# Performance work log

Measured on AMD Instinct MI355X. Metric: run time of the kernel, lower is better.

## Reference

```python
import jax, jax.numpy as jnp
import numpy as np

H = 6  # hidden size == input size

def setup_inputs() -> dict:
    key = jax.random.key(0)
    ks = jax.random.split(key, 14)
    B, T = 8192, 512
    s_in = 1.0 / np.sqrt(H)
    inp = {
        "x": jax.random.normal(ks[0], (B, T, H), dtype=jnp.float32),
        # PyTorch LSTM param layout: w_ih [4H, in], w_hh [4H, H], gate order i,f,g,o
        "w_ih_0": jax.random.uniform(ks[1], (4 * H, H), jnp.float32, -s_in, s_in),
        "w_hh_0": jax.random.uniform(ks[2], (4 * H, H), jnp.float32, -s_in, s_in),
        "b_ih_0": jax.random.uniform(ks[3], (4 * H,), jnp.float32, -s_in, s_in),
        "b_hh_0": jax.random.uniform(ks[4], (4 * H,), jnp.float32, -s_in, s_in),
        "w_ih_1": jax.random.uniform(ks[5], (4 * H, H), jnp.float32, -s_in, s_in),
        "w_hh_1": jax.random.uniform(ks[6], (4 * H, H), jnp.float32, -s_in, s_in),
        "b_ih_1": jax.random.uniform(ks[7], (4 * H,), jnp.float32, -s_in, s_in),
        "b_hh_1": jax.random.uniform(ks[8], (4 * H,), jnp.float32, -s_in, s_in),
        "fc1_w": jax.random.uniform(ks[9], (32, H), jnp.float32, -s_in, s_in),
        "fc1_b": jax.random.uniform(ks[10], (32,), jnp.float32, -s_in, s_in),
        "fc2_w": jax.random.uniform(ks[11], (1, 32), jnp.float32, -1 / np.sqrt(32), 1 / np.sqrt(32)),
        "fc2_b": jax.random.uniform(ks[12], (1,), jnp.float32, -1 / np.sqrt(32), 1 / np.sqrt(32)),
    }
    return inp


def _lstm_cell(x_t, h, c, w_ih, w_hh, b):
    # gates: [B, 4H]; PyTorch order i, f, g, o
    gates = x_t @ w_ih.T + h @ w_hh.T + b
    i, f, g, o = jnp.split(gates, 4, axis=-1)
    i = jax.nn.sigmoid(i)
    f = jax.nn.sigmoid(f)
    g = jnp.tanh(g)
    o = jax.nn.sigmoid(o)
    c_new = f * c + i * g
    h_new = o * jnp.tanh(c_new)
    return h_new, c_new


def reference(x, w_ih_0, w_hh_0, b_ih_0, b_hh_0, w_ih_1, w_hh_1, b_ih_1, b_hh_1,
              fc1_w, fc1_b, fc2_w, fc2_b):
    B, T, _ = x.shape
    b0 = b_ih_0 + b_hh_0
    b1 = b_ih_1 + b_hh_1
    zeros = jnp.zeros((B, H), dtype=x.dtype)

    def step(carry, x_t):
        h0, c0, h1, c1 = carry
        h0, c0 = _lstm_cell(x_t, h0, c0, w_ih_0, w_hh_0, b0)
        h1, c1 = _lstm_cell(h0, h1, c1, w_ih_1, w_hh_1, b1)
        return (h0, c0, h1, c1), h1

    xs = jnp.swapaxes(x, 0, 1)  # [T, B, H]
    _, ys = jax.lax.scan(step, (zeros, zeros, zeros, zeros), xs)
    out = jnp.swapaxes(ys, 0, 1)  # [B, T, H]

    # eval-mode: dropout is identity
    out = jax.nn.relu(out @ fc1_w.T + fc1_b)
    out = jax.nn.relu(out @ fc2_w.T + fc2_b)
    return out  # [B, T, 1]
```

## Files before the change

### kernel.cpp

```cpp
#include <hip/hip_runtime.h>


typedef float v2f __attribute__((ext_vector_type(2)));

static constexpr float L2E  = 1.44269504088896340736f;
static constexpr float TL2E = 2.0f * L2E;

#define DPP_QP(a,b,c,d) ((a)|((b)<<2)|((c)<<4)|((d)<<6))
#define DPP_X1  DPP_QP(1,0,3,2)
#define DPP_X2  DPP_QP(2,3,0,1)
#define DPP_B0  DPP_QP(0,0,0,0)
#define DPP_B1  DPP_QP(1,1,1,1)
#define DPP_B2  DPP_QP(2,2,2,2)
#define DPP_B3  DPP_QP(3,3,3,3)
#define DPP_X8  0x128

template<int CTRL>
__device__ __forceinline__ float dppf(float v) {
    return __int_as_float(__builtin_amdgcn_update_dpp(
        0, __float_as_int(v), CTRL, 0xF, 0xF, true));
}

#define PIN(v) asm volatile("" : "+v"(v))

#define PKFMA_LO(d,a,b) asm("v_pk_fma_f32 %0, %1, %2, %0 op_sel:[0,0,0] op_sel_hi:[1,0,1]" : "+v"(d) : "v"(a), "v"(b))
#define PKFMA_HI(d,a,b) asm("v_pk_fma_f32 %0, %1, %2, %0 op_sel:[0,1,0] op_sel_hi:[1,1,1]" : "+v"(d) : "v"(a), "v"(b))
#define PKADD(d,a,b)    asm("v_pk_add_f32 %0, %1, %2" : "=v"(d) : "v"(a), "v"(b))

__device__ __forceinline__ float sig_pre(float a) {
    return __builtin_amdgcn_rcpf(1.0f + __builtin_amdgcn_exp2f(a));
}
__device__ __forceinline__ float tanh_pre(float a) {
    return fmaf(-2.0f, __builtin_amdgcn_rcpf(1.0f + __builtin_amdgcn_exp2f(a)), 1.0f);
}

extern "C" __global__ void __launch_bounds__(64)
__attribute__((amdgpu_waves_per_eu(1, 1)))
lstm_dpp8v6(const float* __restrict__ x,
            const float* __restrict__ wih0, const float* __restrict__ whh0,
            const float* __restrict__ bih0, const float* __restrict__ bhh0,
            const float* __restrict__ wih1, const float* __restrict__ whh1,
            const float* __restrict__ bih1, const float* __restrict__ bhh1,
            const float* __restrict__ fc1w, const float* __restrict__ fc1b,
            const float* __restrict__ fc2w, const float* __restrict__ fc2b,
            float* __restrict__ out, int nbatch)
{
    const int L   = threadIdx.x;
    const int l   = L & 15;
    const int row = L >> 4;
    const int cst = (l >> 2) & 1;
    const int p   = (l & 3) | ((l >> 3) << 2);
    const bool lowq = ((L >> 3) & 1) == 0;

    int seq = blockIdx.x * 8 + row * 2 + cst;
    const bool live = (seq < nbatch);
    if (!live) seq = nbatch - 1;

    const float km = (p < 6) ? 1.0f : 0.0f;
    const int   k  = (p < 6) ? p : 0;
    const int ir = k, fr = 6 + k, gr = 12 + k, orr = 18 + k;

    v2f wiA0[6], wiB0[6];
    v2f whA0[6], whB0[6], wiA1[6], wiB1[6], whA1[6], whB1[6], f1wA[6], f1wB[6];
#pragma unroll
    for (int j = 0; j < 6; ++j) {
        wiA0[j] = (v2f){ wih0[ir*6+j]*(-L2E)*km,  wih0[fr*6+j]*(-L2E)*km };
        wiB0[j] = (v2f){ wih0[gr*6+j]*( TL2E)*km, wih0[orr*6+j]*(-L2E)*km };
        whA0[j] = (v2f){ whh0[ir*6+j]*(-L2E)*km,  whh0[fr*6+j]*(-L2E)*km };
        whB0[j] = (v2f){ whh0[gr*6+j]*( TL2E)*km, whh0[orr*6+j]*(-L2E)*km };
        wiA1[j] = (v2f){ wih1[ir*6+j]*(-L2E)*km,  wih1[fr*6+j]*(-L2E)*km };
        wiB1[j] = (v2f){ wih1[gr*6+j]*( TL2E)*km, wih1[orr*6+j]*(-L2E)*km };
        whA1[j] = (v2f){ whh1[ir*6+j]*(-L2E)*km,  whh1[fr*6+j]*(-L2E)*km };
        whB1[j] = (v2f){ whh1[gr*6+j]*( TL2E)*km, whh1[orr*6+j]*(-L2E)*km };
        f1wA[j] = (v2f){ fc1w[(4*p+0)*6+j], fc1w[(4*p+1)*6+j] };
        f1wB[j] = (v2f){ fc1w[(4*p+2)*6+j], fc1w[(4*p+3)*6+j] };
    }
    v2f bbA0 = (v2f){ (bih0[ir]+bhh0[ir])*(-L2E)*km,  (bih0[fr]+bhh0[fr])*(-L2E)*km };
    v2f bbB0 = (v2f){ (bih0[gr]+bhh0[gr])*( TL2E)*km, (bih0[orr]+bhh0[orr])*(-L2E)*km };
    v2f bbA1 = (v2f){ (bih1[ir]+bhh1[ir])*(-L2E)*km,  (bih1[fr]+bhh1[fr])*(-L2E)*km };
    v2f bbB1 = (v2f){ (bih1[gr]+bhh1[gr])*( TL2E)*km, (bih1[orr]+bhh1[orr])*(-L2E)*km };
    v2f f1bA = (v2f){ fc1b[4*p+0], fc1b[4*p+1] };
    v2f f1bB = (v2f){ fc1b[4*p+2], fc1b[4*p+3] };
    v2f f2wA = (v2f){ fc2w[4*p+0], fc2w[4*p+1] };
    v2f f2wB = (v2f){ fc2w[4*p+2], fc2w[4*p+3] };
    float f2b = fc2b[0];

#pragma unroll
    for (int j = 0; j < 6; ++j) {
        PIN(wiA0[j]); PIN(wiB0[j]); PIN(whA0[j]); PIN(whB0[j]);
        PIN(wiA1[j]); PIN(wiB1[j]); PIN(whA1[j]); PIN(whB1[j]);
        PIN(f1wA[j]); PIN(f1wB[j]);
    }
    PIN(bbA0); PIN(bbB0); PIN(bbA1); PIN(bbB1);
    PIN(f1bA); PIN(f1bB); PIN(f2wA); PIN(f2wB); PIN(f2b);

    v2f h0p[3], h1p[3];
    const v2f Z2 = (v2f){0.0f, 0.0f};
#pragma unroll
    for (int q = 0; q < 3; ++q) { h0p[q] = Z2; h1p[q] = Z2; }
    float c0 = 0.0f, c1 = 0.0f;

    const float* xp = x + (size_t)seq * (512 * 6);
    float*       op = out + (size_t)seq * 512;

    v2f xq[4][3];
#pragma unroll
    for (int j = 0; j < 4; ++j) {
        const float* q = xp + j * 6;
        xq[j][0] = *(const v2f*)(q + 0);
        xq[j][1] = *(const v2f*)(q + 2);
        xq[j][2] = *(const v2f*)(q + 4);
    }

#define GATHER(HP_, HV_)                                                        \
    {                                                                           \
        float u_ = dppf<DPP_X8>(HV_);                     \
        float hl = lowq ? (HV_) : u_;                 \
        float hh = lowq ? u_ : (HV_);                 \
        HP_[0] = (v2f){ dppf<DPP_B0>(hl), dppf<DPP_B1>(hl) };                   \
        HP_[1] = (v2f){ dppf<DPP_B2>(hl), dppf<DPP_B3>(hl) };                   \
        HP_[2] = (v2f){ dppf<DPP_B0>(hh), dppf<DPP_B1>(hh) };                   \
    }

    float y[4];

    for (int T = 0; T < 512; T += 4) {
        const int Tn = (T < 508) ? T + 4 : 508;
#pragma unroll
        for (int j = 0; j < 4; ++j) {
            const float* xr = xp + (Tn + j) * 6;
            v2f nx0 = *(const v2f*)(xr + 0);
            v2f nx1 = *(const v2f*)(xr + 2);
            v2f nx2 = *(const v2f*)(xr + 4);

            v2f pA = bbA1, pA2 = Z2, pB = bbB1, pB2 = Z2;
            PKFMA_LO(pA, whA1[0], h1p[0]); PKFMA_HI(pA2, whA1[1], h1p[0]);
            PKFMA_LO(pA, whA1[2], h1p[1]); PKFMA_HI(pA2, whA1[3], h1p[1]);
            PKFMA_LO(pA, whA1[4], h1p[2]); PKFMA_HI(pA2, whA1[5], h1p[2]);
            PKFMA_LO(pB, whB1[0], h1p[0]); PKFMA_HI(pB2, whB1[1], h1p[0]);
            PKFMA_LO(pB, whB1[2], h1p[1]); PKFMA_HI(pB2, whB1[3], h1p[1]);
            PKFMA_LO(pB, whB1[4], h1p[2]); PKFMA_HI(pB2, whB1[5], h1p[2]);

            v2f aA = bbA0, aA2 = Z2, aB = bbB0, aB2 = Z2;
            PKFMA_LO(aA, wiA0[0], xq[j][0]); PKFMA_HI(aA2, wiA0[1], xq[j][0]);
            PKFMA_LO(aA, wiA0[2], xq[j][1]); PKFMA_HI(aA2, wiA0[3], xq[j][1]);
            PKFMA_LO(aA, wiA0[4], xq[j][2]); PKFMA_HI(aA2, wiA0[5], xq[j][2]);
            PKFMA_LO(aB, wiB0[0], xq[j][0]); PKFMA_HI(aB2, wiB0[1], xq[j][0]);
            PKFMA_LO(aB, wiB0[2], xq[j][1]); PKFMA_HI(aB2, wiB0[3], xq[j][1]);
            PKFMA_LO(aB, wiB0[4], xq[j][2]); PKFMA_HI(aB2, wiB0[5], xq[j][2]);
            PKFMA_LO(aA, whA0[0], h0p[0]);  PKFMA_HI(aA2, whA0[1], h0p[0]);
            PKFMA_LO(aA, whA0[2], h0p[1]);  PKFMA_HI(aA2, whA0[3], h0p[1]);
            PKFMA_LO(aA, whA0[4], h0p[2]);  PKFMA_HI(aA2, whA0[5], h0p[2]);
            PKFMA_LO(aB, whB0[0], h0p[0]);  PKFMA_HI(aB2, whB0[1], h0p[0]);
            PKFMA_LO(aB, whB0[2], h0p[1]);  PKFMA_HI(aB2, whB0[3], h0p[1]);
            PKFMA_LO(aB, whB0[4], h0p[2]);  PKFMA_HI(aB2, whB0[5], h0p[2]);
            v2f gA0, gB0;
            PKADD(gA0, aA, aA2);
            PKADD(gB0, aB, aB2);

            float i0 = sig_pre(gA0.x), f0 = sig_pre(gA0.y);
            float g0 = tanh_pre(gB0.x), o0 = sig_pre(gB0.y);
            c0 = fmaf(f0, c0, i0 * g0);
            float h0 = o0 * tanh_pre(TL2E * c0);

            GATHER(h0p, h0);

            PKFMA_LO(pA, wiA1[0], h0p[0]); PKFMA_HI(pA2, wiA1[1], h0p[0]);
            PKFMA_LO(pA, wiA1[2], h0p[1]); PKFMA_HI(pA2, wiA1[3], h0p[1]);
            PKFMA_LO(pA, wiA1[4], h0p[2]); PKFMA_HI(pA2, wiA1[5], h0p[2]);
            PKFMA_LO(pB, wiB1[0], h0p[0]); PKFMA_HI(pB2, wiB1[1], h0p[0]);
            PKFMA_LO(pB, wiB1[2], h0p[1]); PKFMA_HI(pB2, wiB1[3], h0p[1]);
            PKFMA_LO(pB, wiB1[4], h0p[2]); PKFMA_HI(pB2, wiB1[5], h0p[2]);
            v2f gA1, gB1;
            PKADD(gA1, pA, pA2);
            PKADD(gB1, pB, pB2);

            float i1 = sig_pre(gA1.x), f1 = sig_pre(gA1.y);
            float g1 = tanh_pre(gB1.x), o1 = sig_pre(gB1.y);
            c1 = fmaf(f1, c1, i1 * g1);
            float h1 = o1 * tanh_pre(TL2E * c1);

            GATHER(h1p, h1);

            v2f rA = f1bA, rA2 = Z2, rB = f1bB, rB2 = Z2;
            PKFMA_LO(rA, f1wA[0], h1p[0]); PKFMA_HI(rA2, f1wA[1], h1p[0]);
            PKFMA_LO(rA, f1wA[2], h1p[1]); PKFMA_HI(rA2, f1wA[3], h1p[1]);
            PKFMA_LO(rA, f1wA[4], h1p[2]); PKFMA_HI(rA2, f1wA[5], h1p[2]);
            PKFMA_LO(rB, f1wB[0], h1p[0]); PKFMA_HI(rB2, f1wB[1], h1p[0]);
            PKFMA_LO(rB, f1wB[2], h1p[1]); PKFMA_HI(rB2, f1wB[3], h1p[1]);
            PKFMA_LO(rB, f1wB[4], h1p[2]); PKFMA_HI(rB2, f1wB[5], h1p[2]);
            v2f RA, RB;
            PKADD(RA, rA, rA2);
            PKADD(RB, rB, rB2);
            float acc =          fmaxf(RA.x, 0.0f) * f2wA.x;
            acc = fmaf(fmaxf(RA.y, 0.0f), f2wA.y, acc);
            acc = fmaf(fmaxf(RB.x, 0.0f), f2wB.x, acc);
            acc = fmaf(fmaxf(RB.y, 0.0f), f2wB.y, acc);
            acc += dppf<DPP_X1>(acc);
            acc += dppf<DPP_X2>(acc);
            acc += dppf<DPP_X8>(acc);
            y[j] = fmaxf(acc + f2b, 0.0f);

            xq[j][0] = nx0; xq[j][1] = nx1; xq[j][2] = nx2;
        }
        if (live && ((L & 11) == 0)) {
            float4 yv = make_float4(y[0], y[1], y[2], y[3]);
            *(float4*)(op + T) = yv;
        }
    }
}

extern "C" void kernel_launch(void* const* d_in, const int* in_sizes, int n_in,
                              void* d_out, int out_size, void* d_ws, size_t ws_size,
                              hipStream_t stream) {
    const float* x     = (const float*)d_in[0];
    const float* wih0  = (const float*)d_in[1];
    const float* whh0  = (const float*)d_in[2];
    const float* bih0  = (const float*)d_in[3];
    const float* bhh0  = (const float*)d_in[4];
    const float* wih1  = (const float*)d_in[5];
    const float* whh1  = (const float*)d_in[6];
    const float* bih1  = (const float*)d_in[7];
    const float* bhh1  = (const float*)d_in[8];
    const float* fc1w  = (const float*)d_in[9];
    const float* fc1b  = (const float*)d_in[10];
    const float* fc2w  = (const float*)d_in[11];
    const float* fc2b  = (const float*)d_in[12];
    float* out = (float*)d_out;

    const int nbatch = in_sizes[0] / (512 * 6);
    const int grid   = (nbatch + 7) / 8;

    hipLaunchKernelGGL(lstm_dpp8v6, dim3(grid), dim3(64), 0, stream,
                       x, wih0, whh0, bih0, bhh0, wih1, whh1, bih1, bhh1,
                       fc1w, fc1b, fc2w, fc2b, out, nbatch);
}
```

Measured before the change: 199.0 us.

## Remap LSTM to 16 lanes per sequence with scalar FMAs and two waves per EU

Each sequence now gets 16 lanes instead of 8. Each half-row of 8 lanes computes two gate rows with scalar FMAs (i/g in one half, f/o in the other), and the other half's gates are exchanged through a DPP row rotate. Packed FMA inline asm is dropped, the fc1 projection is spread across 16 lanes with two outputs each, and the time unroll drops from 4 to 2. The grid doubles and the occupancy hint rises to 2 waves per EU to hide latency. In exchange each step's serial dependency chain gets longer because of the extra DPP exchanges, and sequences per wave are halved.

```diff
diff --git a/kernel.cpp b/kernel.cpp
--- a/kernel.cpp
+++ b/kernel.cpp
@@ -7,13 +7,15 @@
 static constexpr float TL2E = 2.0f * L2E;
 
 #define DPP_QP(a,b,c,d) ((a)|((b)<<2)|((c)<<4)|((d)<<6))
-#define DPP_X1  DPP_QP(1,0,3,2)
-#define DPP_X2  DPP_QP(2,3,0,1)
 #define DPP_B0  DPP_QP(0,0,0,0)
 #define DPP_B1  DPP_QP(1,1,1,1)
 #define DPP_B2  DPP_QP(2,2,2,2)
 #define DPP_B3  DPP_QP(3,3,3,3)
-#define DPP_X8  0x128
+#define DPP_R1  0x121
+#define DPP_R2  0x122
+#define DPP_R4  0x124
+#define DPP_R8  0x128
+#define DPP_R12 0x12C
 
 template<int CTRL>
 __device__ __forceinline__ float dppf(float v) {
@@ -23,191 +25,176 @@
 
 #define PIN(v) asm volatile("" : "+v"(v))
 
-#define PKFMA_LO(d,a,b) asm("v_pk_fma_f32 %0, %1, %2, %0 op_sel:[0,0,0] op_sel_hi:[1,0,1]" : "+v"(d) : "v"(a), "v"(b))
-#define PKFMA_HI(d,a,b) asm("v_pk_fma_f32 %0, %1, %2, %0 op_sel:[0,1,0] op_sel_hi:[1,1,1]" : "+v"(d) : "v"(a), "v"(b))
-#define PKADD(d,a,b)    asm("v_pk_add_f32 %0, %1, %2" : "=v"(d) : "v"(a), "v"(b))
-
-__device__ __forceinline__ float sig_pre(float a) {
-    return __builtin_amdgcn_rcpf(1.0f + __builtin_amdgcn_exp2f(a));
-}
-__device__ __forceinline__ float tanh_pre(float a) {
-    return fmaf(-2.0f, __builtin_amdgcn_rcpf(1.0f + __builtin_amdgcn_exp2f(a)), 1.0f);
+__device__ __forceinline__ float act_pre(float a, float negB) {
+    return fmaf(negB, __builtin_amdgcn_rcpf(1.0f + __builtin_amdgcn_exp2f(a)), 1.0f);
 }
 
 extern "C" __global__ void __launch_bounds__(64)
-__attribute__((amdgpu_waves_per_eu(1, 1)))
-lstm_dpp8v6(const float* __restrict__ x,
-            const float* __restrict__ wih0, const float* __restrict__ whh0,
-            const float* __restrict__ bih0, const float* __restrict__ bhh0,
-            const float* __restrict__ wih1, const float* __restrict__ whh1,
-            const float* __restrict__ bih1, const float* __restrict__ bhh1,
-            const float* __restrict__ fc1w, const float* __restrict__ fc1b,
-            const float* __restrict__ fc2w, const float* __restrict__ fc2b,
-            float* __restrict__ out, int nbatch)
+__attribute__((amdgpu_waves_per_eu(2, 2)))
+lstm16dpp(const float* __restrict__ x,
+          const float* __restrict__ wih0, const float* __restrict__ whh0,
+          const float* __restrict__ bih0, const float* __restrict__ bhh0,
+          const float* __restrict__ wih1, const float* __restrict__ whh1,
+          const float* __restrict__ bih1, const float* __restrict__ bhh1,
+          const float* __restrict__ fc1w, const float* __restrict__ fc1b,
+          const float* __restrict__ fc2w, const float* __restrict__ fc2b,
+          float* __restrict__ out, int nbatch)
 {
-    const int L   = threadIdx.x;
-    const int l   = L & 15;
-    const int row = L >> 4;
-    const int cst = (l >> 2) & 1;
-    const int p   = (l & 3) | ((l >> 3) << 2);
-    const bool lowq = ((L >> 3) & 1) == 0;
-
-    int seq = blockIdx.x * 8 + row * 2 + cst;
-    const bool live = (seq < nbatch);
-    if (!live) seq = nbatch - 1;
-
-    const float km = (p < 6) ? 1.0f : 0.0f;
-    const int   k  = (p < 6) ? p : 0;
-    const int ir = k, fr = 6 + k, gr = 12 + k, orr = 18 + k;
-
-    v2f wiA0[6], wiB0[6];
-    v2f whA0[6], whB0[6], wiA1[6], wiB1[6], whA1[6], whB1[6], f1wA[6], f1wB[6];
+    const int L    = threadIdx.x;
+    const int l    = L & 15;
+    const int half = l >> 3;
+    const int k    = l & 7;
+    const bool qe  = ((l >> 2) & 1) == 0;
+
+    int seq = blockIdx.x * 4 + (L >> 4);
+    if (seq >= nbatch) seq = nbatch - 1;
+
+    const float km = (k < 6) ? 1.0f : 0.0f;
+    const int   kk = (k < 6) ? k : 0;
+
+    const int r1 = (half ? 12 : 0) + kk;
+    const int r2 = (half ? 18 : 6) + kk;
+    const float s1 = km * (half ? TL2E : L2E);
+    const float s2 = km * L2E;
+    const float negB1 = half ? -2.0f : -1.0f;
+
+    float wi0a[6], wi0b[6], wh0a[6], wh0b[6];
+    float wi1a[6], wi1b[6], wh1a[6], wh1b[6];
 #pragma unroll
     for (int j = 0; j < 6; ++j) {
-        wiA0[j] = (v2f){ wih0[ir*6+j]*(-L2E)*km,  wih0[fr*6+j]*(-L2E)*km };
-        wiB0[j] = (v2f){ wih0[gr*6+j]*( TL2E)*km, wih0[orr*6+j]*(-L2E)*km };
-        whA0[j] = (v2f){ whh0[ir*6+j]*(-L2E)*km,  whh0[fr*6+j]*(-L2E)*km };
-        whB0[j] = (v2f){ whh0[gr*6+j]*( TL2E)*km, whh0[orr*6+j]*(-L2E)*km };
-        wiA1[j] = (v2f){ wih1[ir*6+j]*(-L2E)*km,  wih1[fr*6+j]*(-L2E)*km };
-        wiB1[j] = (v2f){ wih1[gr*6+j]*( TL2E)*km, wih1[orr*6+j]*(-L2E)*km };
-        whA1[j] = (v2f){ whh1[ir*6+j]*(-L2E)*km,  whh1[fr*6+j]*(-L2E)*km };
-        whB1[j] = (v2f){ whh1[gr*6+j]*( TL2E)*km, whh1[orr*6+j]*(-L2E)*km };
-        f1wA[j] = (v2f){ fc1w[(4*p+0)*6+j], fc1w[(4*p+1)*6+j] };
-        f1wB[j] = (v2f){ fc1w[(4*p+2)*6+j], fc1w[(4*p+3)*6+j] };
-    }
-    v2f bbA0 = (v2f){ (bih0[ir]+bhh0[ir])*(-L2E)*km,  (bih0[fr]+bhh0[fr])*(-L2E)*km };
-    v2f bbB0 = (v2f){ (bih0[gr]+bhh0[gr])*( TL2E)*km, (bih0[orr]+bhh0[orr])*(-L2E)*km };
-    v2f bbA1 = (v2f){ (bih1[ir]+bhh1[ir])*(-L2E)*km,  (bih1[fr]+bhh1[fr])*(-L2E)*km };
-    v2f bbB1 = (v2f){ (bih1[gr]+bhh1[gr])*( TL2E)*km, (bih1[orr]+bhh1[orr])*(-L2E)*km };
-    v2f f1bA = (v2f){ fc1b[4*p+0], fc1b[4*p+1] };
-    v2f f1bB = (v2f){ fc1b[4*p+2], fc1b[4*p+3] };
-    v2f f2wA = (v2f){ fc2w[4*p+0], fc2w[4*p+1] };
-    v2f f2wB = (v2f){ fc2w[4*p+2], fc2w[4*p+3] };
-    float f2b = fc2b[0];
-
+        wi0a[j] = wih0[r1 * 6 + j] * s1;  wi0b[j] = wih0[r2 * 6 + j] * s2;
+        wh0a[j] = whh0[r1 * 6 + j] * s1;  wh0b[j] = whh0[r2 * 6 + j] * s2;
+        wi1a[j] = wih1[r1 * 6 + j] * s1;  wi1b[j] = wih1[r2 * 6 + j] * s2;
+        wh1a[j] = whh1[r1 * 6 + j] * s1;  wh1b[j] = whh1[r2 * 6 + j] * s2;
+    }
+    float b0a = (bih0[r1] + bhh0[r1]) * s1, b0b = (bih0[r2] + bhh0[r2]) * s2;
+    float b1a = (bih1[r1] + bhh1[r1]) * s1, b1b = (bih1[r2] + bhh1[r2]) * s2;
+
+    float fwA[6], fwB[6];
 #pragma unroll
     for (int j = 0; j < 6; ++j) {
-        PIN(wiA0[j]); PIN(wiB0[j]); PIN(whA0[j]); PIN(whB0[j]);
-        PIN(wiA1[j]); PIN(wiB1[j]); PIN(whA1[j]); PIN(whB1[j]);
-        PIN(f1wA[j]); PIN(f1wB[j]);
-    }
-    PIN(bbA0); PIN(bbB0); PIN(bbA1); PIN(bbB1);
-    PIN(f1bA); PIN(f1bB); PIN(f2wA); PIN(f2wB); PIN(f2b);
-
-    v2f h0p[3], h1p[3];
-    const v2f Z2 = (v2f){0.0f, 0.0f};
-#pragma unroll
-    for (int q = 0; q < 3; ++q) { h0p[q] = Z2; h1p[q] = Z2; }
+        fwA[j] = fc1w[(2 * l    ) * 6 + j];
+        fwB[j] = fc1w[(2 * l + 1) * 6 + j];
+    }
+    float fbA = fc1b[2 * l], fbB = fc1b[2 * l + 1];
+    float f2A = fc2w[2 * l], f2B = fc2w[2 * l + 1];
+    const float f2b = fc2b[0];
+
+#pragma unroll
+    for (int j = 0; j < 6; ++j) {
+        PIN(wi0a[j]); PIN(wi0b[j]); PIN(wh0a[j]); PIN(wh0b[j]);
+        PIN(wi1a[j]); PIN(wi1b[j]); PIN(wh1a[j]); PIN(wh1b[j]);
+        PIN(fwA[j]);  PIN(fwB[j]);
+    }
+    PIN(b0a); PIN(b0b); PIN(b1a); PIN(b1b);
+    PIN(fbA); PIN(fbB); PIN(f2A); PIN(f2B);
+
+    float h0u[6], h1u[6];
+#pragma unroll
+    for (int j = 0; j < 6; ++j) { h0u[j] = 0.0f; h1u[j] = 0.0f; }
     float c0 = 0.0f, c1 = 0.0f;
 
-    const float* xp = x + (size_t)seq * (512 * 6);
+    const float* xp = x + (size_t)seq * 3072;
     float*       op = out + (size_t)seq * 512;
 
-    v2f xq[4][3];
-#pragma unroll
-    for (int j = 0; j < 4; ++j) {
-        const float* q = xp + j * 6;
-        xq[j][0] = *(const v2f*)(q + 0);
-        xq[j][1] = *(const v2f*)(q + 2);
-        xq[j][2] = *(const v2f*)(q + 4);
-    }
-
-#define GATHER(HP_, HV_)                                                        \
+    v2f xqA[3], xqB[3];
+    xqA[0] = *(const v2f*)(xp + 0); xqA[1] = *(const v2f*)(xp + 2); xqA[2] = *(const v2f*)(xp + 4);
+    xqB[0] = *(const v2f*)(xp + 6); xqB[1] = *(const v2f*)(xp + 8); xqB[2] = *(const v2f*)(xp + 10);
+
+#define GATHER(HU_, HV_)                                    \
+    {                                                       \
+        float u_  = dppf<DPP_R12>(HV_);                     \
+        float hl_ = qe ? (HV_) : u_;                        \
+        float hh_ = qe ? u_ : (HV_);                        \
+        HU_[0] = dppf<DPP_B0>(hl_);                         \
+        HU_[1] = dppf<DPP_B1>(hl_);                         \
+        HU_[2] = dppf<DPP_B2>(hl_);                         \
+        HU_[3] = dppf<DPP_B3>(hl_);                         \
+        HU_[4] = dppf<DPP_B0>(hh_);                         \
+        HU_[5] = dppf<DPP_B1>(hh_);                         \
+    }
+
+#define STEP(XC_, TP_, YV_)                                                     \
     {                                                                           \
-        float u_ = dppf<DPP_X8>(HV_);                     \
-        float hl = lowq ? (HV_) : u_;                 \
-        float hh = lowq ? u_ : (HV_);                 \
-        HP_[0] = (v2f){ dppf<DPP_B0>(hl), dppf<DPP_B1>(hl) };                   \
-        HP_[1] = (v2f){ dppf<DPP_B2>(hl), dppf<DPP_B3>(hl) };                   \
-        HP_[2] = (v2f){ dppf<DPP_B0>(hh), dppf<DPP_B1>(hh) };                   \
-    }
-
-    float y[4];
-
-    for (int T = 0; T < 512; T += 4) {
-        const int Tn = (T < 508) ? T + 4 : 508;
-#pragma unroll
-        for (int j = 0; j < 4; ++j) {
-            const float* xr = xp + (Tn + j) * 6;
-            v2f nx0 = *(const v2f*)(xr + 0);
-            v2f nx1 = *(const v2f*)(xr + 2);
-            v2f nx2 = *(const v2f*)(xr + 4);
-
-            v2f pA = bbA1, pA2 = Z2, pB = bbB1, pB2 = Z2;
-            PKFMA_LO(pA, whA1[0], h1p[0]); PKFMA_HI(pA2, whA1[1], h1p[0]);
-            PKFMA_LO(pA, whA1[2], h1p[1]); PKFMA_HI(pA2, whA1[3], h1p[1]);
-            PKFMA_LO(pA, whA1[4], h1p[2]); PKFMA_HI(pA2, whA1[5], h1p[2]);
-            PKFMA_LO(pB, whB1[0], h1p[0]); PKFMA_HI(pB2, whB1[1], h1p[0]);
-            PKFMA_LO(pB, whB1[2], h1p[1]); PKFMA_HI(pB2, whB1[3], h1p[1]);
-            PKFMA_LO(pB, whB1[4], h1p[2]); PKFMA_HI(pB2, whB1[5], h1p[2]);
-
-            v2f aA = bbA0, aA2 = Z2, aB = bbB0, aB2 = Z2;
-            PKFMA_LO(aA, wiA0[0], xq[j][0]); PKFMA_HI(aA2, wiA0[1], xq[j][0]);
-            PKFMA_LO(aA, wiA0[2], xq[j][1]); PKFMA_HI(aA2, wiA0[3], xq[j][1]);
-            PKFMA_LO(aA, wiA0[4], xq[j][2]); PKFMA_HI(aA2, wiA0[5], xq[j][2]);
-            PKFMA_LO(aB, wiB0[0], xq[j][0]); PKFMA_HI(aB2, wiB0[1], xq[j][0]);
-            PKFMA_LO(aB, wiB0[2], xq[j][1]); PKFMA_HI(aB2, wiB0[3], xq[j][1]);
-            PKFMA_LO(aB, wiB0[4], xq[j][2]); PKFMA_HI(aB2, wiB0[5], xq[j][2]);
-            PKFMA_LO(aA, whA0[0], h0p[0]);  PKFMA_HI(aA2, whA0[1], h0p[0]);
-            PKFMA_LO(aA, whA0[2], h0p[1]);  PKFMA_HI(aA2, whA0[3], h0p[1]);
-            PKFMA_LO(aA, whA0[4], h0p[2]);  PKFMA_HI(aA2, whA0[5], h0p[2]);
-            PKFMA_LO(aB, whB0[0], h0p[0]);  PKFMA_HI(aB2, whB0[1], h0p[0]);
-            PKFMA_LO(aB, whB0[2], h0p[1]);  PKFMA_HI(aB2, whB0[3], h0p[1]);
-            PKFMA_LO(aB, whB0[4], h0p[2]);  PKFMA_HI(aB2, whB0[5], h0p[2]);
-            v2f gA0, gB0;
-            PKADD(gA0, aA, aA2);
-            PKADD(gB0, aB, aB2);
-
-            float i0 = sig_pre(gA0.x), f0 = sig_pre(gA0.y);
-            float g0 = tanh_pre(gB0.x), o0 = sig_pre(gB0.y);
-            c0 = fmaf(f0, c0, i0 * g0);
-            float h0 = o0 * tanh_pre(TL2E * c0);
-
-            GATHER(h0p, h0);
-
-            PKFMA_LO(pA, wiA1[0], h0p[0]); PKFMA_HI(pA2, wiA1[1], h0p[0]);
-            PKFMA_LO(pA, wiA1[2], h0p[1]); PKFMA_HI(pA2, wiA1[3], h0p[1]);
-            PKFMA_LO(pA, wiA1[4], h0p[2]); PKFMA_HI(pA2, wiA1[5], h0p[2]);
-            PKFMA_LO(pB, wiB1[0], h0p[0]); PKFMA_HI(pB2, wiB1[1], h0p[0]);
-            PKFMA_LO(pB, wiB1[2], h0p[1]); PKFMA_HI(pB2, wiB1[3], h0p[1]);
-            PKFMA_LO(pB, wiB1[4], h0p[2]); PKFMA_HI(pB2, wiB1[5], h0p[2]);
-            v2f gA1, gB1;
-            PKADD(gA1, pA, pA2);
-            PKADD(gB1, pB, pB2);
-
-            float i1 = sig_pre(gA1.x), f1 = sig_pre(gA1.y);
-            float g1 = tanh_pre(gB1.x), o1 = sig_pre(gB1.y);
-            c1 = fmaf(f1, c1, i1 * g1);
-            float h1 = o1 * tanh_pre(TL2E * c1);
-
-            GATHER(h1p, h1);
-
-            v2f rA = f1bA, rA2 = Z2, rB = f1bB, rB2 = Z2;
-            PKFMA_LO(rA, f1wA[0], h1p[0]); PKFMA_HI(rA2, f1wA[1], h1p[0]);
-            PKFMA_LO(rA, f1wA[2], h1p[1]); PKFMA_HI(rA2, f1wA[3], h1p[1]);
-            PKFMA_LO(rA, f1wA[4], h1p[2]); PKFMA_HI(rA2, f1wA[5], h1p[2]);
-            PKFMA_LO(rB, f1wB[0], h1p[0]); PKFMA_HI(rB2, f1wB[1], h1p[0]);
-            PKFMA_LO(rB, f1wB[2], h1p[1]); PKFMA_HI(rB2, f1wB[3], h1p[1]);
-            PKFMA_LO(rB, f1wB[4], h1p[2]); PKFMA_HI(rB2, f1wB[5], h1p[2]);
-            v2f RA, RB;
-            PKADD(RA, rA, rA2);
-            PKADD(RB, rB, rB2);
-            float acc =          fmaxf(RA.x, 0.0f) * f2wA.x;
-            acc = fmaf(fmaxf(RA.y, 0.0f), f2wA.y, acc);
-            acc = fmaf(fmaxf(RB.x, 0.0f), f2wB.x, acc);
-            acc = fmaf(fmaxf(RB.y, 0.0f), f2wB.y, acc);
-            acc += dppf<DPP_X1>(acc);
-            acc += dppf<DPP_X2>(acc);
-            acc += dppf<DPP_X8>(acc);
-            y[j] = fmaxf(acc + f2b, 0.0f);
-
-            xq[j][0] = nx0; xq[j][1] = nx1; xq[j][2] = nx2;
-        }
-        if (live && ((L & 11) == 0)) {
-            float4 yv = make_float4(y[0], y[1], y[2], y[3]);
-            *(float4*)(op + T) = yv;
-        }
-    }
+                      \
+        const float* xr_ = xp + (TP_) * 6;                                      \
+        v2f nx0_ = *(const v2f*)(xr_ + 0);                                      \
+        v2f nx1_ = *(const v2f*)(xr_ + 2);                                      \
+        v2f nx2_ = *(const v2f*)(xr_ + 4);                                      \
+              \
+        float p1a_ = b1a, p1b_ = b1b, q1a_ = 0.0f, q1b_ = 0.0f;                 \
+        p1a_ = fmaf(wh1a[0], h1u[0], p1a_); q1a_ = fmaf(wh1a[1], h1u[1], q1a_); \
+        p1a_ = fmaf(wh1a[2], h1u[2], p1a_); q1a_ = fmaf(wh1a[3], h1u[3], q1a_); \
+        p1a_ = fmaf(wh1a[4], h1u[4], p1a_); q1a_ = fmaf(wh1a[5], h1u[5], q1a_); \
+        p1b_ = fmaf(wh1b[0], h1u[0], p1b_); q1b_ = fmaf(wh1b[1], h1u[1], q1b_); \
+        p1b_ = fmaf(wh1b[2], h1u[2], p1b_); q1b_ = fmaf(wh1b[3], h1u[3], q1b_); \
+        p1b_ = fmaf(wh1b[4], h1u[4], p1b_); q1b_ = fmaf(wh1b[5], h1u[5], q1b_); \
+                          \
+        float a0a_ = b0a, a0b_ = b0b, z0a_ = 0.0f, z0b_ = 0.0f;                 \
+        a0a_ = fmaf(wi0a[0], XC_[0].x, a0a_); z0a_ = fmaf(wi0a[1], XC_[0].y, z0a_); \
+        a0a_ = fmaf(wi0a[2], XC_[1].x, a0a_); z0a_ = fmaf(wi0a[3], XC_[1].y, z0a_); \
+        a0a_ = fmaf(wi0a[4], XC_[2].x, a0a_); z0a_ = fmaf(wi0a[5], XC_[2].y, z0a_); \
+        a0b_ = fmaf(wi0b[0], XC_[0].x, a0b_); z0b_ = fmaf(wi0b[1], XC_[0].y, z0b_); \
+        a0b_ = fmaf(wi0b[2], XC_[1].x, a0b_); z0b_ = fmaf(wi0b[3], XC_[1].y, z0b_); \
+        a0b_ = fmaf(wi0b[4], XC_[2].x, a0b_); z0b_ = fmaf(wi0b[5], XC_[2].y, z0b_); \
+        a0a_ = fmaf(wh0a[0], h0u[0], a0a_); z0a_ = fmaf(wh0a[1], h0u[1], z0a_); \
+        a0a_ = fmaf(wh0a[2], h0u[2], a0a_); z0a_ = fmaf(wh0a[3], h0u[3], z0a_); \
+        a0a_ = fmaf(wh0a[4], h0u[4], a0a_); z0a_ = fmaf(wh0a[5], h0u[5], z0a_); \
+        a0b_ = fmaf(wh0b[0], h0u[0], a0b_); z0b_ = fmaf(wh0b[1], h0u[1], z0b_); \
+        a0b_ = fmaf(wh0b[2], h0u[2], a0b_); z0b_ = fmaf(wh0b[3], h0u[3], z0b_); \
+        a0b_ = fmaf(wh0b[4], h0u[4], a0b_); z0b_ = fmaf(wh0b[5], h0u[5], z0b_); \
+        float A1_ = act_pre(a0a_ + z0a_, negB1);     \
+        float A2_ = act_pre(a0b_ + z0b_, -1.0f);     \
+        float S1_ = dppf<DPP_R8>(A1_);                                          \
+        float S2_ = dppf<DPP_R8>(A2_);                                          \
+        float fv_ = half ? S2_ : A2_;                                           \
+        float ov_ = half ? A2_ : S2_;                                           \
+        c0 = fmaf(fv_, c0, A1_ * S1_);              \
+        float h0_ = ov_ * act_pre(TL2E * c0, -2.0f);                            \
+        GATHER(h0u, h0_);                                                       \
+                                   \
+        p1a_ = fmaf(wi1a[0], h0u[0], p1a_); q1a_ = fmaf(wi1a[1], h0u[1], q1a_); \
+        p1a_ = fmaf(wi1a[2], h0u[2], p1a_); q1a_ = fmaf(wi1a[3], h0u[3], q1a_); \
+        p1a_ = fmaf(wi1a[4], h0u[4], p1a_); q1a_ = fmaf(wi1a[5], h0u[5], q1a_); \
+        p1b_ = fmaf(wi1b[0], h0u[0], p1b_); q1b_ = fmaf(wi1b[1], h0u[1], q1b_); \
+        p1b_ = fmaf(wi1b[2], h0u[2], p1b_); q1b_ = fmaf(wi1b[3], h0u[3], q1b_); \
+        p1b_ = fmaf(wi1b[4], h0u[4], p1b_); q1b_ = fmaf(wi1b[5], h0u[5], q1b_); \
+        float B1_ = act_pre(p1a_ + q1a_, negB1);                                \
+        float B2_ = act_pre(p1b_ + q1b_, -1.0f);                                \
+        float T1_ = dppf<DPP_R8>(B1_);                                          \
+        float T2_ = dppf<DPP_R8>(B2_);                                          \
+        float fw_ = half ? T2_ : B2_;                                           \
+        float ow_ = half ? B2_ : T2_;                                           \
+        c1 = fmaf(fw_, c1, B1_ * T1_);                                          \
+        float h1_ = ow_ * act_pre(TL2E * c1, -2.0f);                            \
+        GATHER(h1u, h1_);                                                       \
+              \
+        float rA_ = fbA, rB_ = fbB;                                             \
+        rA_ = fmaf(fwA[0], h1u[0], rA_); rB_ = fmaf(fwB[0], h1u[0], rB_);       \
+        rA_ = fmaf(fwA[1], h1u[1], rA_); rB_ = fmaf(fwB[1], h1u[1], rB_);       \
+        rA_ = fmaf(fwA[2], h1u[2], rA_); rB_ = fmaf(fwB[2], h1u[2], rB_);       \
+        rA_ = fmaf(fwA[3], h1u[3], rA_); rB_ = fmaf(fwB[3], h1u[3], rB_);       \
+        rA_ = fmaf(fwA[4], h1u[4], rA_); rB_ = fmaf(fwB[4], h1u[4], rB_);       \
+        rA_ = fmaf(fwA[5], h1u[5], rA_); rB_ = fmaf(fwB[5], h1u[5], rB_);       \
+        float acc_ = fmaxf(rA_, 0.0f) * f2A;                                    \
+        acc_ = fmaf(fmaxf(rB_, 0.0f), f2B, acc_);                               \
+        acc_ += dppf<DPP_R1>(acc_);                                             \
+        acc_ += dppf<DPP_R2>(acc_);                                             \
+        acc_ += dppf<DPP_R4>(acc_);                                             \
+        acc_ += dppf<DPP_R8>(acc_);                                             \
+        YV_ = fmaxf(acc_ + f2b, 0.0f);                                          \
+                                            \
+        XC_[0] = nx0_; XC_[1] = nx1_; XC_[2] = nx2_;                            \
+    }
+
+    for (int t = 0; t < 512; t += 2) {
+        float y0_, y1_;
+        STEP(xqA, (t + 2 < 512 ? t + 2 : 510), y0_);
+        STEP(xqB, (t + 3 < 512 ? t + 3 : 511), y1_);
+        if ((L & 15) == 0) *(float2*)(op + t) = make_float2(y0_, y1_);
+    }
+#undef STEP
+#undef GATHER
 }
 
 extern "C" void kernel_launch(void* const* d_in, const int* in_sizes, int n_in,
@@ -229,9 +216,9 @@
     float* out = (float*)d_out;
 
     const int nbatch = in_sizes[0] / (512 * 6);
-    const int grid   = (nbatch + 7) / 8;
-
-    hipLaunchKernelGGL(lstm_dpp8v6, dim3(grid), dim3(64), 0, stream,
+    const int grid   = (nbatch + 3) / 4;
+
+    hipLaunchKernelGGL(lstm16dpp, dim3(grid), dim3(64), 0, stream,
                        x, wih0, whh0, bih0, bhh0, wih1, whh1, bih1, bhh1,
                        fc1w, fc1b, fc2w, fc2b, out, nbatch);
 }
```

Result: slower. 259.4 us (+30.4%).

## Precompute next-step input projection off the critical path and use software reciprocal in activations

Applied to the files above, without the earlier changes.

Layer-0 input-to-gate products for the next timestep are now computed during the current step's activation phase. The recurrent dependency chain then only contains the hidden-state FMAs. Sigmoid and tanh now use a sign-split exp2 with a polynomial-plus-Newton reciprocal instead of the hardware rcp, so more work runs on regular FMA lanes instead of the transcendental unit. The trade-off is extra VALU instructions, a longer dependent chain inside each activation, and a few more live registers.

```diff
diff --git a/kernel.cpp b/kernel.cpp
--- a/kernel.cpp
+++ b/kernel.cpp
@@ -27,16 +27,27 @@
 #define PKFMA_HI(d,a,b) asm("v_pk_fma_f32 %0, %1, %2, %0 op_sel:[0,1,0] op_sel_hi:[1,1,1]" : "+v"(d) : "v"(a), "v"(b))
 #define PKADD(d,a,b)    asm("v_pk_add_f32 %0, %1, %2" : "=v"(d) : "v"(a), "v"(b))
 
-__device__ __forceinline__ float sig_pre(float a) {
-    return __builtin_amdgcn_rcpf(1.0f + __builtin_amdgcn_exp2f(a));
-}
+__device__ __forceinline__ float rcp1p(float e) {
+    float y = 1.0f + e;
+    float r = fmaf(y, fmaf(y, 0.32559f, -1.46518f), 2.13186f);
+    r = r * fmaf(-y, r, 2.0f);
+    r = r * fmaf(-y, r, 2.0f);
+    return r;
+}
+__device__ __forceinline__ float sig2(float a) {
+    float e = __builtin_amdgcn_exp2f(-fabsf(a));
+    float r = rcp1p(e);
+    float m = (a <= 0.0f) ? 1.0f : e;
+    return r * m;
+}
+__device__ __forceinline__ float sig_pre(float a) { return sig2(a); }
 __device__ __forceinline__ float tanh_pre(float a) {
-    return fmaf(-2.0f, __builtin_amdgcn_rcpf(1.0f + __builtin_amdgcn_exp2f(a)), 1.0f);
+    return fmaf(-2.0f, sig2(a), 1.0f);
 }
 
 extern "C" __global__ void __launch_bounds__(64)
 __attribute__((amdgpu_waves_per_eu(1, 1)))
-lstm_dpp8v6(const float* __restrict__ x,
+lstm_dpp8v8(const float* __restrict__ x,
             const float* __restrict__ wih0, const float* __restrict__ whh0,
             const float* __restrict__ bih0, const float* __restrict__ bhh0,
             const float* __restrict__ wih1, const float* __restrict__ whh1,
@@ -122,6 +133,17 @@
         HP_[2] = (v2f){ dppf<DPP_B0>(hh), dppf<DPP_B1>(hh) };                   \
     }
 
+    v2f xgA, xgA2, xgB, xgB2;
+    {
+        xgA = bbA0; xgA2 = Z2; xgB = bbB0; xgB2 = Z2;
+        PKFMA_LO(xgA, wiA0[0], xq[0][0]); PKFMA_HI(xgA2, wiA0[1], xq[0][0]);
+        PKFMA_LO(xgA, wiA0[2], xq[0][1]); PKFMA_HI(xgA2, wiA0[3], xq[0][1]);
+        PKFMA_LO(xgA, wiA0[4], xq[0][2]); PKFMA_HI(xgA2, wiA0[5], xq[0][2]);
+        PKFMA_LO(xgB, wiB0[0], xq[0][0]); PKFMA_HI(xgB2, wiB0[1], xq[0][0]);
+        PKFMA_LO(xgB, wiB0[2], xq[0][1]); PKFMA_HI(xgB2, wiB0[3], xq[0][1]);
+        PKFMA_LO(xgB, wiB0[4], xq[0][2]); PKFMA_HI(xgB2, wiB0[5], xq[0][2]);
+    }
+
     float y[4];
 
     for (int T = 0; T < 512; T += 4) {
@@ -141,13 +163,7 @@
             PKFMA_LO(pB, whB1[2], h1p[1]); PKFMA_HI(pB2, whB1[3], h1p[1]);
             PKFMA_LO(pB, whB1[4], h1p[2]); PKFMA_HI(pB2, whB1[5], h1p[2]);
 
-            v2f aA = bbA0, aA2 = Z2, aB = bbB0, aB2 = Z2;
-            PKFMA_LO(aA, wiA0[0], xq[j][0]); PKFMA_HI(aA2, wiA0[1], xq[j][0]);
-            PKFMA_LO(aA, wiA0[2], xq[j][1]); PKFMA_HI(aA2, wiA0[3], xq[j][1]);
-            PKFMA_LO(aA, wiA0[4], xq[j][2]); PKFMA_HI(aA2, wiA0[5], xq[j][2]);
-            PKFMA_LO(aB, wiB0[0], xq[j][0]); PKFMA_HI(aB2, wiB0[1], xq[j][0]);
-            PKFMA_LO(aB, wiB0[2], xq[j][1]); PKFMA_HI(aB2, wiB0[3], xq[j][1]);
-            PKFMA_LO(aB, wiB0[4], xq[j][2]); PKFMA_HI(aB2, wiB0[5], xq[j][2]);
+            v2f aA = xgA, aA2 = xgA2, aB = xgB, aB2 = xgB2;
             PKFMA_LO(aA, whA0[0], h0p[0]);  PKFMA_HI(aA2, whA0[1], h0p[0]);
             PKFMA_LO(aA, whA0[2], h0p[1]);  PKFMA_HI(aA2, whA0[3], h0p[1]);
             PKFMA_LO(aA, whA0[4], h0p[2]);  PKFMA_HI(aA2, whA0[5], h0p[2]);
@@ -160,6 +176,19 @@
 
             float i0 = sig_pre(gA0.x), f0 = sig_pre(gA0.y);
             float g0 = tanh_pre(gB0.x), o0 = sig_pre(gB0.y);
+
+            {
+                const v2f* xn = xq[(j + 1) & 3];
+                v2f tA = bbA0, tA2 = Z2, tB = bbB0, tB2 = Z2;
+                PKFMA_LO(tA, wiA0[0], xn[0]); PKFMA_HI(tA2, wiA0[1], xn[0]);
+                PKFMA_LO(tA, wiA0[2], xn[1]); PKFMA_HI(tA2, wiA0[3], xn[1]);
+                PKFMA_LO(tA, wiA0[4], xn[2]); PKFMA_HI(tA2, wiA0[5], xn[2]);
+                PKFMA_LO(tB, wiB0[0], xn[0]); PKFMA_HI(tB2, wiB0[1], xn[0]);
+                PKFMA_LO(tB, wiB0[2], xn[1]); PKFMA_HI(tB2, wiB0[3], xn[1]);
+                PKFMA_LO(tB, wiB0[4], xn[2]); PKFMA_HI(tB2, wiB0[5], xn[2]);
+                xgA = tA; xgA2 = tA2; xgB = tB; xgB2 = tB2;
+            }
+
             c0 = fmaf(f0, c0, i0 * g0);
             float h0 = o0 * tanh_pre(TL2E * c0);
 
@@ -231,7 +260,7 @@
     const int nbatch = in_sizes[0] / (512 * 6);
     const int grid   = (nbatch + 7) / 8;
 
-    hipLaunchKernelGGL(lstm_dpp8v6, dim3(grid), dim3(64), 0, stream,
+    hipLaunchKernelGGL(lstm_dpp8v8, dim3(grid), dim3(64), 0, stream,
                        x, wih0, whh0, bih0, bhh0, wih1, whh1, bih1, bhh1,
                        fc1w, fc1b, fc2w, fc2b, out, nbatch);
 }
```

New measurement: 242.6 us. +21.9%, slower.

## Software-pipeline LSTM layers so layer 0 runs one timestep ahead of layer 1

Applied to the files above, without the earlier changes.

Restructures the recurrence so each iteration computes layer-1 gates for step t while layer-0 gate pre-activations and exps for step t+1 are produced in the same body. The two dependency chains then interleave instead of running strictly in series, which is meant to hide transcendental and DPP latency on the critical path. A prologue, a peeled epilogue and a deeper x prefetch (six steps ahead) are added, which raises register pressure and code size.

```diff
diff --git a/kernel.cpp b/kernel.cpp
--- a/kernel.cpp
+++ b/kernel.cpp
@@ -27,8 +27,16 @@
 #define PKFMA_HI(d,a,b) asm("v_pk_fma_f32 %0, %1, %2, %0 op_sel:[0,1,0] op_sel_hi:[1,1,1]" : "+v"(d) : "v"(a), "v"(b))
 #define PKADD(d,a,b)    asm("v_pk_add_f32 %0, %1, %2" : "=v"(d) : "v"(a), "v"(b))
 
-__device__ __forceinline__ float sig_pre(float a) {
-    return __builtin_amdgcn_rcpf(1.0f + __builtin_amdgcn_exp2f(a));
+#define ACC12(DST_, DST2_, W_, S_)                              \
+    PKFMA_LO(DST_, W_[0], S_[0]); PKFMA_HI(DST2_, W_[1], S_[0]); \
+    PKFMA_LO(DST_, W_[2], S_[1]); PKFMA_HI(DST2_, W_[3], S_[1]); \
+    PKFMA_LO(DST_, W_[4], S_[2]); PKFMA_HI(DST2_, W_[5], S_[2])
+
+__device__ __forceinline__ float sig_from_e(float e) {
+    return __builtin_amdgcn_rcpf(1.0f + e);
+}
+__device__ __forceinline__ float tanh_from_e(float e) {
+    return fmaf(-2.0f, __builtin_amdgcn_rcpf(1.0f + e), 1.0f);
 }
 __device__ __forceinline__ float tanh_pre(float a) {
     return fmaf(-2.0f, __builtin_amdgcn_rcpf(1.0f + __builtin_amdgcn_exp2f(a)), 1.0f);
@@ -36,14 +44,14 @@
 
 extern "C" __global__ void __launch_bounds__(64)
 __attribute__((amdgpu_waves_per_eu(1, 1)))
-lstm_dpp8v6(const float* __restrict__ x,
-            const float* __restrict__ wih0, const float* __restrict__ whh0,
-            const float* __restrict__ bih0, const float* __restrict__ bhh0,
-            const float* __restrict__ wih1, const float* __restrict__ whh1,
-            const float* __restrict__ bih1, const float* __restrict__ bhh1,
-            const float* __restrict__ fc1w, const float* __restrict__ fc1b,
-            const float* __restrict__ fc2w, const float* __restrict__ fc2b,
-            float* __restrict__ out, int nbatch)
+lstm_dpp8v14(const float* __restrict__ x,
+             const float* __restrict__ wih0, const float* __restrict__ whh0,
+             const float* __restrict__ bih0, const float* __restrict__ bhh0,
+             const float* __restrict__ wih1, const float* __restrict__ whh1,
+             const float* __restrict__ bih1, const float* __restrict__ bhh1,
+             const float* __restrict__ fc1w, const float* __restrict__ fc1b,
+             const float* __restrict__ fc2w, const float* __restrict__ fc2b,
+             float* __restrict__ out, int nbatch)
 {
     const int L   = threadIdx.x;
     const int l   = L & 15;
@@ -103,111 +111,155 @@
     const float* xp = x + (size_t)seq * (512 * 6);
     float*       op = out + (size_t)seq * 512;
 
+#define GATHER(HP_, HV_)                                                        \
+    {                                                                           \
+        float u_ = dppf<DPP_X8>(HV_);                                           \
+        float hl = lowq ? (HV_) : u_;                                           \
+        float hh = lowq ? u_ : (HV_);                                           \
+        HP_[0] = (v2f){ dppf<DPP_B0>(hl), dppf<DPP_B1>(hl) };                   \
+        HP_[1] = (v2f){ dppf<DPP_B2>(hl), dppf<DPP_B3>(hl) };                   \
+        HP_[2] = (v2f){ dppf<DPP_B0>(hh), dppf<DPP_B1>(hh) };                   \
+    }
+
+    float exi, exf, exg, exo;
+
+#define CLOSE0()                                                                \
+    {                                                                           \
+        v2f gA0n, gB0n;                                                         \
+        PKADD(gA0n, xgA, xgA2);                                                 \
+        PKADD(gB0n, xgB, xgB2);                                                 \
+        exi = __builtin_amdgcn_exp2f(gA0n.x);                                   \
+        exf = __builtin_amdgcn_exp2f(gA0n.y);                                   \
+        exg = __builtin_amdgcn_exp2f(gB0n.x);                                   \
+        exo = __builtin_amdgcn_exp2f(gB0n.y);                                   \
+    }
+
+    v2f xgA, xgA2, xgB, xgB2;
+
+    {
+        v2f x0[3], x1[3];
+        x0[0] = *(const v2f*)(xp + 0); x0[1] = *(const v2f*)(xp + 2); x0[2] = *(const v2f*)(xp + 4);
+        x1[0] = *(const v2f*)(xp + 6); x1[1] = *(const v2f*)(xp + 8); x1[2] = *(const v2f*)(xp + 10);
+        xgA = bbA0; xgA2 = Z2; xgB = bbB0; xgB2 = Z2;
+        ACC12(xgA, xgA2, wiA0, x0);
+        ACC12(xgB, xgB2, wiB0, x0);
+        CLOSE0();
+        float i0 = sig_from_e(exi), f0 = sig_from_e(exf);
+        float g0 = tanh_from_e(exg), o0 = sig_from_e(exo);
+        c0 = fmaf(f0, c0, i0 * g0);
+        float h0_ = o0 * tanh_pre(TL2E * c0);
+        GATHER(h0p, h0_);
+        xgA = bbA0; xgA2 = Z2; xgB = bbB0; xgB2 = Z2;
+        ACC12(xgA, xgA2, wiA0, x1);
+        ACC12(xgB, xgB2, wiB0, x1);
+        ACC12(xgA, xgA2, whA0, h0p);
+        ACC12(xgB, xgB2, whB0, h0p);
+        CLOSE0();
+    }
+
     v2f xq[4][3];
 #pragma unroll
     for (int j = 0; j < 4; ++j) {
-        const float* q = xp + j * 6;
+        const float* q = xp + (j + 2) * 6;
         xq[j][0] = *(const v2f*)(q + 0);
         xq[j][1] = *(const v2f*)(q + 2);
         xq[j][2] = *(const v2f*)(q + 4);
     }
 
-#define GATHER(HP_, HV_)                                                        \
+#define BODY(XC1_, PF_, DOPF_, DOB_, DOC_, YDST_)                               \
     {                                                                           \
-        float u_ = dppf<DPP_X8>(HV_);                     \
-        float hl = lowq ? (HV_) : u_;                 \
-        float hh = lowq ? u_ : (HV_);                 \
-        HP_[0] = (v2f){ dppf<DPP_B0>(hl), dppf<DPP_B1>(hl) };                   \
-        HP_[1] = (v2f){ dppf<DPP_B2>(hl), dppf<DPP_B3>(hl) };                   \
-        HP_[2] = (v2f){ dppf<DPP_B0>(hh), dppf<DPP_B1>(hh) };                   \
+        v2f nx0 = Z2, nx1 = Z2, nx2 = Z2;                                       \
+        if (DOPF_) {                                                            \
+            const float* xr_ = xp + (PF_) * 6;                                  \
+            nx0 = *(const v2f*)(xr_ + 0);                                       \
+            nx1 = *(const v2f*)(xr_ + 2);                                       \
+            nx2 = *(const v2f*)(xr_ + 4);                                       \
+        }                                                                       \
+                 \
+        v2f pA = bbA1, pA2 = Z2, pB = bbB1, pB2 = Z2;                           \
+        ACC12(pA, pA2, whA1, h1p);                                              \
+        ACC12(pB, pB2, whB1, h1p);                                              \
+        ACC12(pA, pA2, wiA1, h0p);                 \
+        ACC12(pB, pB2, wiB1, h0p);                                              \
+        v2f gA1, gB1;                                                           \
+        PKADD(gA1, pA, pA2);                                                    \
+        PKADD(gB1, pB, pB2);                                                    \
+        float e1i = __builtin_amdgcn_exp2f(gA1.x);                              \
+        float e1f = __builtin_amdgcn_exp2f(gA1.y);                              \
+        float e1g = __builtin_amdgcn_exp2f(gB1.x);                              \
+        float e1o = __builtin_amdgcn_exp2f(gB1.y);                              \
+                                             \
+        if (DOB_) {                                                             \
+            float i0 = sig_from_e(exi), f0 = sig_from_e(exf);                   \
+            float g0 = tanh_from_e(exg), o0 = sig_from_e(exo);                  \
+            c0 = fmaf(f0, c0, i0 * g0);                                         \
+            float h0_ = o0 * tanh_pre(TL2E * c0);                               \
+            GATHER(h0p, h0_);                                                   \
+        }                                                                       \
+                                            \
+        float i1 = sig_from_e(e1i), f1 = sig_from_e(e1f);                       \
+        float g1 = tanh_from_e(e1g), o1 = sig_from_e(e1o);                      \
+        c1 = fmaf(f1, c1, i1 * g1);                                             \
+        float h1_ = o1 * tanh_pre(TL2E * c1);                                   \
+        GATHER(h1p, h1_);                                                       \
+                  \
+        if (DOC_) {                                                             \
+            xgA = bbA0; xgA2 = Z2; xgB = bbB0; xgB2 = Z2;                       \
+            ACC12(xgA, xgA2, wiA0, XC1_);                                       \
+            ACC12(xgB, xgB2, wiB0, XC1_);                                       \
+            ACC12(xgA, xgA2, whA0, h0p);                                        \
+            ACC12(xgB, xgB2, whB0, h0p);                                        \
+            CLOSE0();                                                           \
+        }                                                                       \
+                                                    \
+        {                                                                       \
+            v2f rA = f1bA, rA2 = Z2, rB = f1bB, rB2 = Z2;                       \
+            ACC12(rA, rA2, f1wA, h1p);                                          \
+            ACC12(rB, rB2, f1wB, h1p);                                          \
+            v2f RA, RB;                                                         \
+            PKADD(RA, rA, rA2);                                                 \
+            PKADD(RB, rB, rB2);                                                 \
+            float acc =          fmaxf(RA.x, 0.0f) * f2wA.x;                    \
+            acc = fmaf(fmaxf(RA.y, 0.0f), f2wA.y, acc);                         \
+            acc = fmaf(fmaxf(RB.x, 0.0f), f2wB.x, acc);                         \
+            acc = fmaf(fmaxf(RB.y, 0.0f), f2wB.y, acc);                         \
+            acc += dppf<DPP_X1>(acc);                                           \
+            acc += dppf<DPP_X2>(acc);                                           \
+            acc += dppf<DPP_X8>(acc);                                           \
+            YDST_ = fmaxf(acc + f2b, 0.0f);                                     \
+        }                                                                       \
+        if (DOPF_) { XC1_[0] = nx0; XC1_[1] = nx1; XC1_[2] = nx2; }             \
     }
 
     float y[4];
 
-    for (int T = 0; T < 512; T += 4) {
-        const int Tn = (T < 508) ? T + 4 : 508;
+    for (int T = 0; T < 508; T += 4) {
 #pragma unroll
         for (int j = 0; j < 4; ++j) {
-            const float* xr = xp + (Tn + j) * 6;
-            v2f nx0 = *(const v2f*)(xr + 0);
-            v2f nx1 = *(const v2f*)(xr + 2);
-            v2f nx2 = *(const v2f*)(xr + 4);
-
-            v2f pA = bbA1, pA2 = Z2, pB = bbB1, pB2 = Z2;
-            PKFMA_LO(pA, whA1[0], h1p[0]); PKFMA_HI(pA2, whA1[1], h1p[0]);
-            PKFMA_LO(pA, whA1[2], h1p[1]); PKFMA_HI(pA2, whA1[3], h1p[1]);
-            PKFMA_LO(pA, whA1[4], h1p[2]); PKFMA_HI(pA2, whA1[5], h1p[2]);
-            PKFMA_LO(pB, whB1[0], h1p[0]); PKFMA_HI(pB2, whB1[1], h1p[0]);
-            PKFMA_LO(pB, whB1[2], h1p[1]); PKFMA_HI(pB2, whB1[3], h1p[1]);
-            PKFMA_LO(pB, whB1[4], h1p[2]); PKFMA_HI(pB2, whB1[5], h1p[2]);
-
-            v2f aA = bbA0, aA2 = Z2, aB = bbB0, aB2 = Z2;
-            PKFMA_LO(aA, wiA0[0], xq[j][0]); PKFMA_HI(aA2, wiA0[1], xq[j][0]);
-            PKFMA_LO(aA, wiA0[2], xq[j][1]); PKFMA_HI(aA2, wiA0[3], xq[j][1]);
-            PKFMA_LO(aA, wiA0[4], xq[j][2]); PKFMA_HI(aA2, wiA0[5], xq[j][2]);
-            PKFMA_LO(aB, wiB0[0], xq[j][0]); PKFMA_HI(aB2, wiB0[1], xq[j][0]);
-            PKFMA_LO(aB, wiB0[2], xq[j][1]); PKFMA_HI(aB2, wiB0[3], xq[j][1]);
-            PKFMA_LO(aB, wiB0[4], xq[j][2]); PKFMA_HI(aB2, wiB0[5], xq[j][2]);
-            PKFMA_LO(aA, whA0[0], h0p[0]);  PKFMA_HI(aA2, whA0[1], h0p[0]);
-            PKFMA_LO(aA, whA0[2], h0p[1]);  PKFMA_HI(aA2, whA0[3], h0p[1]);
-            PKFMA_LO(aA, whA0[4], h0p[2]);  PKFMA_HI(aA2, whA0[5], h0p[2]);
-            PKFMA_LO(aB, whB0[0], h0p[0]);  PKFMA_HI(aB2, whB0[1], h0p[0]);
-            PKFMA_LO(aB, whB0[2], h0p[1]);  PKFMA_HI(aB2, whB0[3], h0p[1]);
-            PKFMA_LO(aB, whB0[4], h0p[2]);  PKFMA_HI(aB2, whB0[5], h0p[2]);
-            v2f gA0, gB0;
-            PKADD(gA0, aA, aA2);
-            PKADD(gB0, aB, aB2);
-
-            float i0 = sig_pre(gA0.x), f0 = sig_pre(gA0.y);
-            float g0 = tanh_pre(gB0.x), o0 = sig_pre(gB0.y);
-            c0 = fmaf(f0, c0, i0 * g0);
-            float h0 = o0 * tanh_pre(TL2E * c0);
-
-            GATHER(h0p, h0);
-
-            PKFMA_LO(pA, wiA1[0], h0p[0]); PKFMA_HI(pA2, wiA1[1], h0p[0]);
-            PKFMA_LO(pA, wiA1[2], h0p[1]); PKFMA_HI(pA2, wiA1[3], h0p[1]);
-            PKFMA_LO(pA, wiA1[4], h0p[2]); PKFMA_HI(pA2, wiA1[5], h0p[2]);
-            PKFMA_LO(pB, wiB1[0], h0p[0]); PKFMA_HI(pB2, wiB1[1], h0p[0]);
-            PKFMA_LO(pB, wiB1[2], h0p[1]); PKFMA_HI(pB2, wiB1[3], h0p[1]);
-            PKFMA_LO(pB, wiB1[4], h0p[2]); PKFMA_HI(pB2, wiB1[5], h0p[2]);
-            v2f gA1, gB1;
-            PKADD(gA1, pA, pA2);
-            PKADD(gB1, pB, pB2);
-
-            float i1 = sig_pre(gA1.x), f1 = sig_pre(gA1.y);
-            float g1 = tanh_pre(gB1.x), o1 = sig_pre(gB1.y);
-            c1 = fmaf(f1, c1, i1 * g1);
-            float h1 = o1 * tanh_pre(TL2E * c1);
-
-            GATHER(h1p, h1);
-
-            v2f rA = f1bA, rA2 = Z2, rB = f1bB, rB2 = Z2;
-            PKFMA_LO(rA, f1wA[0], h1p[0]); PKFMA_HI(rA2, f1wA[1], h1p[0]);
-            PKFMA_LO(rA, f1wA[2], h1p[1]); PKFMA_HI(rA2, f1wA[3], h1p[1]);
-            PKFMA_LO(rA, f1wA[4], h1p[2]); PKFMA_HI(rA2, f1wA[5], h1p[2]);
-            PKFMA_LO(rB, f1wB[0], h1p[0]); PKFMA_HI(rB2, f1wB[1], h1p[0]);
-            PKFMA_LO(rB, f1wB[2], h1p[1]); PKFMA_HI(rB2, f1wB[3], h1p[1]);
-            PKFMA_LO(rB, f1wB[4], h1p[2]); PKFMA_HI(rB2, f1wB[5], h1p[2]);
-            v2f RA, RB;
-            PKADD(RA, rA, rA2);
-            PKADD(RB, rB, rB2);
-            float acc =          fmaxf(RA.x, 0.0f) * f2wA.x;
-            acc = fmaf(fmaxf(RA.y, 0.0f), f2wA.y, acc);
-            acc = fmaf(fmaxf(RB.x, 0.0f), f2wB.x, acc);
-            acc = fmaf(fmaxf(RB.y, 0.0f), f2wB.y, acc);
-            acc += dppf<DPP_X1>(acc);
-            acc += dppf<DPP_X2>(acc);
-            acc += dppf<DPP_X8>(acc);
-            y[j] = fmaxf(acc + f2b, 0.0f);
-
-            xq[j][0] = nx0; xq[j][1] = nx1; xq[j][2] = nx2;
+            int pf = T + j + 6;
+            if (pf > 511) pf = 511;
+            BODY(xq[j], pf, true, true, true, y[j]);
         }
         if (live && ((L & 11) == 0)) {
             float4 yv = make_float4(y[0], y[1], y[2], y[3]);
             *(float4*)(op + T) = yv;
         }
     }
+
+    {
+        float yp0, yp1, yp2, yp3;
+        BODY(xq[0], 511, false, true, true,  yp0);
+        BODY(xq[1], 511, false, true, true,  yp1);
+        BODY(xq[2], 511, false, true, false, yp2);
+        BODY(xq[3], 511, false, false, false, yp3);
+        if (live && ((L & 11) == 0)) {
+            float4 yv = make_float4(yp0, yp1, yp2, yp3);
+            *(float4*)(op + 508) = yv;
+        }
+    }
+#undef BODY
+#undef GATHER
+#undef CLOSE0
 }
 
 extern "C" void kernel_launch(void* const* d_in, const int* in_sizes, int n_in,
@@ -231,7 +283,7 @@
     const int nbatch = in_sizes[0] / (512 * 6);
     const int grid   = (nbatch + 7) / 8;
 
-    hipLaunchKernelGGL(lstm_dpp8v6, dim3(grid), dim3(64), 0, stream,
+    hipLaunchKernelGGL(lstm_dpp8v14, dim3(grid), dim3(64), 0, stream,
                        x, wih0, whh0, bih0, bhh0, wih1, whh1, bih1, bhh1,
                        fc1w, fc1b, fc2w, fc2b, out, nbatch);
 }
```

Result: faster. 186.5 us (-6.3%).
